# Kernel tuning notes

Hardware: AMD Instinct MI355X
Metric: run time of the kernel (lower is better)

Reference implementation:

```python
import jax, jax.numpy as jnp
import numpy as np

T, B, D, H = 512, 64, 256, 256


def setup_inputs() -> dict:
    key = jax.random.key(0)
    ks = jax.random.split(key, 14)
    w = lambda k, shp: (0.01 * jax.random.normal(k, shp, dtype=jnp.float32))
    return {
        "X": jax.random.normal(ks[0], (T, B, D), dtype=jnp.float32),
        "Wa_x": w(ks[1], (D, H)), "Wi_x": w(ks[2], (D, H)),
        "Wf_x": w(ks[3], (D, H)), "Wo_x": w(ks[4], (D, H)),
        "Wa_h": w(ks[5], (H, H)), "Wi_h": w(ks[6], (H, H)),
        "Wf_h": w(ks[7], (H, H)), "Wo_h": w(ks[8], (H, H)),
        "ba": w(ks[9], (H,)), "bi": w(ks[10], (H,)),
        "bf": w(ks[11], (H,)), "bo": w(ks[12], (H,)),
    }


def reference(X, Wa_x, Wi_x, Wf_x, Wo_x, Wa_h, Wi_h, Wf_h, Wo_h, ba, bi, bf, bo):
    # Fuse the four gate input projections into one big GEMM over all timesteps.
    # Gate order: a (cell candidate, tanh), i, f, o (sigmoid).
    h_dim = Wa_h.shape[0]
    Wx = jnp.concatenate([Wa_x, Wi_x, Wf_x, Wo_x], axis=1)      # [D, 4H]
    Wh = jnp.concatenate([Wa_h, Wi_h, Wf_h, Wo_h], axis=1)      # [H, 4H]
    b = jnp.concatenate([ba, bi, bf, bo])                        # [4H]
    gx = jnp.einsum('tbd,dg->tbg', X, Wx) + b                    # [T, B, 4H]

    def step(carry, g):
        h, s = carry
        g = g + h @ Wh                                           # [B, 4H]
        a = jnp.tanh(g[:, :h_dim])
        i = jax.nn.sigmoid(g[:, h_dim:2 * h_dim])
        f = jax.nn.sigmoid(g[:, 2 * h_dim:3 * h_dim])
        o = jax.nn.sigmoid(g[:, 3 * h_dim:])
        # t==0 in the original omits h/s terms, equivalent to h0 = s0 = 0
        s = a * i + s * f
        h = jnp.tanh(s) * o
        return (h, s), h

    bsz = X.shape[1]
    h0 = jnp.zeros((bsz, h_dim), dtype=X.dtype)
    s0 = jnp.zeros((bsz, h_dim), dtype=X.dtype)
    _, outputs = jax.lax.scan(step, (h0, s0), gx)                # [T, B, H]
    return outputs
```

## Files before the change

### kernel.cpp

```cpp
#include <hip/hip_runtime.h>
#include <hip/hip_fp16.h>


#define T_STEPS 512
#define BATCH   64
#define HID     256
#define G4      1024
#define GM      (T_STEPS * BATCH)

typedef _Float16 half2_t __attribute__((ext_vector_type(2)));
typedef _Float16 f16x8   __attribute__((ext_vector_type(8)));
typedef float    f32x4   __attribute__((ext_vector_type(4)));

#define XH_OFF  0u
#define WXT_OFF 8388608u
#define GX_OFF  8912896u
#define WH8_BYTE_OFF (8650752u * 2u)

__device__ __forceinline__ float fast_sigmoid(float x) {
    return 1.0f / (1.0f + __expf(-x));
}
__device__ __forceinline__ float fast_tanh(float x) {
    return 2.0f / (1.0f + __expf(-2.0f * x)) - 1.0f;
}

__device__ __forceinline__ unsigned char sw_e4m3(float x) {
    unsigned u = __float_as_uint(x);
    unsigned s = (u >> 24) & 0x80u;
    int e = (int)((u >> 23) & 0xffu) - 127;
    unsigned m = u & 0x7fffffu;
    if (e < -6) return (unsigned char)s;
    m += 0x00080000u;
    if (m & 0x800000u) { m = 0; e += 1; }
    int E = e + 7;
    if (E > 15 || (E == 15 && (m >> 20) > 6)) { E = 15; m = 6u << 20; }
    return (unsigned char)(s | ((unsigned)E << 3) | (m >> 20));
}
template <bool HI>
__device__ __forceinline__ unsigned cvt2_fp8(float a, float b, unsigned old) {
#if __has_builtin(__builtin_amdgcn_cvt_pk_fp8_f32)
    return (unsigned)__builtin_amdgcn_cvt_pk_fp8_f32(a, b, (int)old, HI);
#else
    unsigned lo16 = (unsigned)sw_e4m3(a) | ((unsigned)sw_e4m3(b) << 8);
    return HI ? ((old & 0xFFFFu) | (lo16 << 16))
              : ((old & 0xFFFF0000u) | lo16);
#endif
}

__global__ __launch_bounds__(256) void k_prep_x(const float* __restrict__ X,
                                                _Float16* __restrict__ Xh) {
    const int i = blockIdx.x * 256 + threadIdx.x;
    float4 v = ((const float4*)X)[i];
    half2_t a; a.x = (_Float16)v.x; a.y = (_Float16)v.y;
    half2_t b; b.x = (_Float16)v.z; b.y = (_Float16)v.w;
    ((half2_t*)Xh)[2 * i]     = a;
    ((half2_t*)Xh)[2 * i + 1] = b;
}

__global__ __launch_bounds__(256) void k_prep_w(
    const float* __restrict__ Wax, const float* __restrict__ Wix,
    const float* __restrict__ Wfx, const float* __restrict__ Wox,
    _Float16* __restrict__ Wxt)
{
    const int id = blockIdx.x * 256 + threadIdx.x;
    const int k  = id >> 10;
    const int c  = id & 1023;
    const int g  = c >> 8;
    const int j  = c & 255;
    const float* src = (g == 0) ? Wax : (g == 1) ? Wix : (g == 2) ? Wfx : Wox;
    Wxt[c * 256 + k] = (_Float16)src[k * 256 + j];
}

__global__ __launch_bounds__(256) void k_prep_wfrag8(
    const float* __restrict__ Wah, const float* __restrict__ Wih,
    const float* __restrict__ Wfh, const float* __restrict__ Woh,
    unsigned char* __restrict__ Wh8)
{
    const int id  = blockIdx.x * 256 + threadIdx.x;
    const int l   = id & 63;
    const int kt  = (id >> 6) & 7;
    const int ntG = id >> 9;
    const int c   = ntG * 16 + (l & 15);
    const int u   = c >> 2;
    const int g   = c & 3;
    const int k0  = kt * 32 + (l >> 4) * 8;
    const float* W = (g == 0) ? Wah : (g == 1) ? Wih : (g == 2) ? Wfh : Woh;
    float v[8];
#pragma unroll
    for (int e = 0; e < 8; ++e)
        v[e] = W[(size_t)(k0 + e) * 256 + u] * 64.0f;
    unsigned lo = cvt2_fp8<false>(v[0], v[1], 0u);
    lo = cvt2_fp8<true>(v[2], v[3], lo);
    unsigned hi = cvt2_fp8<false>(v[4], v[5], 0u);
    hi = cvt2_fp8<true>(v[6], v[7], hi);
    uint2 pk; pk.x = lo; pk.y = hi;
    *(uint2*)(Wh8 + ((size_t)(ntG * 8 + kt) * 64 + l) * 8) = pk;
}

__global__ __launch_bounds__(256) void k_gemm(const _Float16* __restrict__ Xh,
                                              const _Float16* __restrict__ Wxt,
                                              const float* __restrict__ ba,
                                              const float* __restrict__ bi,
                                              const float* __restrict__ bf_,
                                              const float* __restrict__ bo,
                                              _Float16* __restrict__ gx)
{
    const int lane = threadIdx.x & 63, wave = threadIdx.x >> 6;
    const int rowbase = blockIdx.x * 128 + wave * 32;
    const int colbase = blockIdx.y * 64;
    const int r15 = lane & 15, kg = lane >> 4;

    f32x4 acc[2][4] = {};
    const _Float16* ap0 = Xh  + (size_t)(rowbase + r15) * 256 + kg * 8;
    const _Float16* ap1 = ap0 + 16 * 256;
    const _Float16* bp  = Wxt + (size_t)(colbase + r15) * 256 + kg * 8;

#pragma unroll
    for (int ks = 0; ks < 8; ++ks) {
        f16x8 a0 = *(const f16x8*)(ap0 + ks * 32);
        f16x8 a1 = *(const f16x8*)(ap1 + ks * 32);
        f16x8 b0 = *(const f16x8*)(bp  + ks * 32);
        f16x8 b1 = *(const f16x8*)(bp  + 16 * 256 + ks * 32);
        f16x8 b2 = *(const f16x8*)(bp  + 32 * 256 + ks * 32);
        f16x8 b3 = *(const f16x8*)(bp  + 48 * 256 + ks * 32);
        acc[0][0] = __builtin_amdgcn_mfma_f32_16x16x32_f16(a0, b0, acc[0][0], 0, 0, 0);
        acc[0][1] = __builtin_amdgcn_mfma_f32_16x16x32_f16(a0, b1, acc[0][1], 0, 0, 0);
        acc[0][2] = __builtin_amdgcn_mfma_f32_16x16x32_f16(a0, b2, acc[0][2], 0, 0, 0);
        acc[0][3] = __builtin_amdgcn_mfma_f32_16x16x32_f16(a0, b3, acc[0][3], 0, 0, 0);
        acc[1][0] = __builtin_amdgcn_mfma_f32_16x16x32_f16(a1, b0, acc[1][0], 0, 0, 0);
        acc[1][1] = __builtin_amdgcn_mfma_f32_16x16x32_f16(a1, b1, acc[1][1], 0, 0, 0);
        acc[1][2] = __builtin_amdgcn_mfma_f32_16x16x32_f16(a1, b2, acc[1][2], 0, 0, 0);
        acc[1][3] = __builtin_amdgcn_mfma_f32_16x16x32_f16(a1, b3, acc[1][3], 0, 0, 0);
    }
    float bias_n[4];
#pragma unroll
    for (int nt = 0; nt < 4; ++nt) {
        int col = colbase + nt * 16 + r15;
        bias_n[nt] = (col < 256) ? ba[col]
                   : (col < 512) ? bi[col - 256]
                   : (col < 768) ? bf_[col - 512]
                                 : bo[col - 768];
    }
#pragma unroll
    for (int mt = 0; mt < 2; ++mt)
#pragma unroll
        for (int nt = 0; nt < 4; ++nt)
#pragma unroll
            for (int r = 0; r < 4; ++r) {
                int row = rowbase + mt * 16 + kg * 4 + r;
                int col = colbase + nt * 16 + r15;
                int g   = col >> 8, j = col & 255;
                gx[(size_t)row * G4 + 4 * j + g] =
                    (_Float16)(acc[mt][nt][r] + bias_n[nt]);
            }
}


#define M8(a, bfr, acc) \
    __builtin_amdgcn_mfma_f32_16x16x32_fp8_fp8((a), (bfr), (acc), 0, 0, 0)
#define WB(n, k) (*(const long*)(Wp + ((size_t)((n) * 8 + (k)) * 64) * 8))

#define DB(n)                                                                  \
    long b##n##_0 = WB(n,0), b##n##_1 = WB(n,1), b##n##_2 = WB(n,2),           \
         b##n##_3 = WB(n,3), b##n##_4 = WB(n,4), b##n##_5 = WB(n,5),           \
         b##n##_6 = WB(n,6), b##n##_7 = WB(n,7);

#define KSTEP(k)                                                               \
    c0  = M8(a##k, b0_##k,  c0);  c1  = M8(a##k, b1_##k,  c1);                 \
    c2  = M8(a##k, b2_##k,  c2);  c3  = M8(a##k, b3_##k,  c3);                 \
    c4  = M8(a##k, b4_##k,  c4);  c5  = M8(a##k, b5_##k,  c5);                 \
    c6  = M8(a##k, b6_##k,  c6);  c7  = M8(a##k, b7_##k,  c7);                 \
    c8  = M8(a##k, b8_##k,  c8);  c9  = M8(a##k, b9_##k,  c9);                 \
    c10 = M8(a##k, b10_##k, c10); c11 = M8(a##k, b11_##k, c11);                \
    c12 = M8(a##k, b12_##k, c12); c13 = M8(a##k, b13_##k, c13);                \
    c14 = M8(a##k, b14_##k, c14); c15 = M8(a##k, b15_##k, c15);

__global__ void __launch_bounds__(256, 1)
__attribute__((amdgpu_waves_per_eu(1, 1)))
k_recur(const unsigned char* __restrict__ Wh8, const _Float16* __restrict__ gx,
        float* __restrict__ out)
{
    const int b    = blockIdx.x;
    const int tid  = threadIdx.x;
    const int lane = tid & 63;
    const int w    = tid >> 6;

    __shared__ __align__(16) float act[1024];
    __shared__ __align__(8)  unsigned char hbufs[2][256];

    float* actw = act + w * 256;
    const unsigned char* Wp = Wh8 + ((size_t)(w * 16) * 8 * 64) * 8 + lane * 8;

    DB(0)  DB(1)  DB(2)  DB(3)  DB(4)  DB(5)  DB(6)  DB(7)
    DB(8)  DB(9)  DB(10) DB(11) DB(12) DB(13) DB(14) DB(15)

    hbufs[0][tid] = 0;
    float s = 0.0f;
    const int u = w * 64 + lane;
    uint2 gcu = *(const uint2*)(gx + (size_t)b * G4 + 4 * u);
    __syncthreads();

#pragma unroll 1
    for (int t = 0; t < T_STEPS; ++t) {
        uint2 gnx; gnx.x = 0u; gnx.y = 0u;
        if (t + 1 < T_STEPS) {
            gnx = *(const uint2*)(gx + ((size_t)(t + 1) * BATCH + b) * G4 + 4 * u);
        }

        const unsigned char* hb = &hbufs[t & 1][0] + ((lane >> 4) * 8);
        long a0 = *(const long*)(hb + 0);
        long a1 = *(const long*)(hb + 32);
        long a2 = *(const long*)(hb + 64);
        long a3 = *(const long*)(hb + 96);
        long a4 = *(const long*)(hb + 128);
        long a5 = *(const long*)(hb + 160);
        long a6 = *(const long*)(hb + 192);
        long a7 = *(const long*)(hb + 224);

        f32x4 c0  = {0,0,0,0}, c1  = {0,0,0,0}, c2  = {0,0,0,0}, c3  = {0,0,0,0};
        f32x4 c4  = {0,0,0,0}, c5  = {0,0,0,0}, c6  = {0,0,0,0}, c7  = {0,0,0,0};
        f32x4 c8  = {0,0,0,0}, c9  = {0,0,0,0}, c10 = {0,0,0,0}, c11 = {0,0,0,0};
        f32x4 c12 = {0,0,0,0}, c13 = {0,0,0,0}, c14 = {0,0,0,0}, c15 = {0,0,0,0};

        KSTEP(0) KSTEP(1) KSTEP(2) KSTEP(3)
        KSTEP(4) KSTEP(5) KSTEP(6) KSTEP(7)

        if (lane < 16) {
            actw[0  * 16 + lane] = c0[0];   actw[1  * 16 + lane] = c1[0];
            actw[2  * 16 + lane] = c2[0];   actw[3  * 16 + lane] = c3[0];
            actw[4  * 16 + lane] = c4[0];   actw[5  * 16 + lane] = c5[0];
            actw[6  * 16 + lane] = c6[0];   actw[7  * 16 + lane] = c7[0];
            actw[8  * 16 + lane] = c8[0];   actw[9  * 16 + lane] = c9[0];
            actw[10 * 16 + lane] = c10[0];  actw[11 * 16 + lane] = c11[0];
            actw[12 * 16 + lane] = c12[0];  actw[13 * 16 + lane] = c13[0];
            actw[14 * 16 + lane] = c14[0];  actw[15 * 16 + lane] = c15[0];
        }
        asm volatile("s_waitcnt lgkmcnt(0)" ::: "memory");

        {
            half2_t p01, p23;
            __builtin_memcpy(&p01, &gcu.x, 4);
            __builtin_memcpy(&p23, &gcu.y, 4);
            float4 g4v = ((const float4*)act)[w * 64 + lane];
            const float S = 0.0009765625f;
            float gA = g4v.x * S + (float)p01.x;
            float gB = g4v.y * S + (float)p01.y;
            float gC = g4v.z * S + (float)p23.x;
            float gD = g4v.w * S + (float)p23.y;
            float aa = fast_tanh(gA);
            float ii = fast_sigmoid(gB);
            float ff = fast_sigmoid(gC);
            float oo = fast_sigmoid(gD);
            s = aa * ii + s * ff;
            float h = fast_tanh(s) * oo;
            out[((size_t)t * BATCH + b) * HID + u] = h;
            unsigned p8 = cvt2_fp8<false>(h * 16.0f, h * 16.0f, 0u);
            hbufs[(t + 1) & 1][u] = (unsigned char)(p8 & 0xffu);
        }
        gcu = gnx;
        __syncthreads();
    }
}

extern "C" void kernel_launch(void* const* d_in, const int* in_sizes, int n_in,
                              void* d_out, int out_size, void* d_ws, size_t ws_size,
                              hipStream_t stream) {
    const float* X   = (const float*)d_in[0];
    const float* Wax = (const float*)d_in[1];
    const float* Wix = (const float*)d_in[2];
    const float* Wfx = (const float*)d_in[3];
    const float* Wox = (const float*)d_in[4];
    const float* Wah = (const float*)d_in[5];
    const float* Wih = (const float*)d_in[6];
    const float* Wfh = (const float*)d_in[7];
    const float* Woh = (const float*)d_in[8];
    const float* ba  = (const float*)d_in[9];
    const float* bi  = (const float*)d_in[10];
    const float* bf  = (const float*)d_in[11];
    const float* bo  = (const float*)d_in[12];

    _Float16* ws  = (_Float16*)d_ws;
    _Float16* Xh  = ws + XH_OFF;
    _Float16* Wxt = ws + WXT_OFF;
    _Float16* gxp = ws + GX_OFF;
    unsigned char* Wh8 = (unsigned char*)d_ws + WH8_BYTE_OFF;

    k_prep_x<<<dim3(GM * 256 / 4 / 256), dim3(256), 0, stream>>>(X, Xh);
    k_prep_w<<<dim3(1024), dim3(256), 0, stream>>>(Wax, Wix, Wfx, Wox, Wxt);
    k_prep_wfrag8<<<dim3(128), dim3(256), 0, stream>>>(Wah, Wih, Wfh, Woh, Wh8);
    k_gemm<<<dim3(GM / 128, G4 / 64), dim3(256), 0, stream>>>(
        Xh, Wxt, ba, bi, bf, bo, gxp);
    k_recur<<<dim3(BATCH), dim3(256), 0, stream>>>(Wh8, gxp, (float*)d_out);
}
```

Before: 929.4 us.

## Split recurrent matvec across eight waves with eight N-tiles each

The recurrent kernel goes from 4 to 8 waves per block. Each wave now holds 8 instead of 16 register-resident FP8 weight tiles and issues half as many MFMAs per timestep, which shortens the serial critical path of each step. The cost is an extra block-wide barrier per step, since gate pre-activations written by one wave are read by threads of another. Only the first 256 threads run the elementwise LSTM update, so half the block idles during that phase.

```diff
diff --git a/kernel.cpp b/kernel.cpp
--- a/kernel.cpp
+++ b/kernel.cpp
@@ -166,17 +166,13 @@
          b##n##_6 = WB(n,6), b##n##_7 = WB(n,7);
 
 #define KSTEP(k)                                                               \
-    c0  = M8(a##k, b0_##k,  c0);  c1  = M8(a##k, b1_##k,  c1);                 \
-    c2  = M8(a##k, b2_##k,  c2);  c3  = M8(a##k, b3_##k,  c3);                 \
-    c4  = M8(a##k, b4_##k,  c4);  c5  = M8(a##k, b5_##k,  c5);                 \
-    c6  = M8(a##k, b6_##k,  c6);  c7  = M8(a##k, b7_##k,  c7);                 \
-    c8  = M8(a##k, b8_##k,  c8);  c9  = M8(a##k, b9_##k,  c9);                 \
-    c10 = M8(a##k, b10_##k, c10); c11 = M8(a##k, b11_##k, c11);                \
-    c12 = M8(a##k, b12_##k, c12); c13 = M8(a##k, b13_##k, c13);                \
-    c14 = M8(a##k, b14_##k, c14); c15 = M8(a##k, b15_##k, c15);
-
-__global__ void __launch_bounds__(256, 1)
-__attribute__((amdgpu_waves_per_eu(1, 1)))
+    c0 = M8(a##k, b0_##k, c0);  c1 = M8(a##k, b1_##k, c1);                     \
+    c2 = M8(a##k, b2_##k, c2);  c3 = M8(a##k, b3_##k, c3);                     \
+    c4 = M8(a##k, b4_##k, c4);  c5 = M8(a##k, b5_##k, c5);                     \
+    c6 = M8(a##k, b6_##k, c6);  c7 = M8(a##k, b7_##k, c7);
+
+__global__ void __launch_bounds__(512, 1)
+__attribute__((amdgpu_waves_per_eu(2, 2)))
 k_recur(const unsigned char* __restrict__ Wh8, const _Float16* __restrict__ gx,
         float* __restrict__ out)
 {
@@ -188,23 +184,22 @@
     __shared__ __align__(16) float act[1024];
     __shared__ __align__(8)  unsigned char hbufs[2][256];
 
-    float* actw = act + w * 256;
-    const unsigned char* Wp = Wh8 + ((size_t)(w * 16) * 8 * 64) * 8 + lane * 8;
-
-    DB(0)  DB(1)  DB(2)  DB(3)  DB(4)  DB(5)  DB(6)  DB(7)
-    DB(8)  DB(9)  DB(10) DB(11) DB(12) DB(13) DB(14) DB(15)
-
-    hbufs[0][tid] = 0;
+    const unsigned char* Wp = Wh8 + ((size_t)(w * 8) * 8 * 64) * 8 + lane * 8;
+
+    DB(0) DB(1) DB(2) DB(3) DB(4) DB(5) DB(6) DB(7)
+
+    if (tid < 256) hbufs[0][tid] = 0;
     float s = 0.0f;
-    const int u = w * 64 + lane;
-    uint2 gcu = *(const uint2*)(gx + (size_t)b * G4 + 4 * u);
+    uint2 gcu; gcu.x = 0u; gcu.y = 0u;
+    if (tid < 256)
+        gcu = *(const uint2*)(gx + (size_t)b * G4 + 4 * tid);
     __syncthreads();
 
 #pragma unroll 1
     for (int t = 0; t < T_STEPS; ++t) {
         uint2 gnx; gnx.x = 0u; gnx.y = 0u;
-        if (t + 1 < T_STEPS) {
-            gnx = *(const uint2*)(gx + ((size_t)(t + 1) * BATCH + b) * G4 + 4 * u);
+        if (tid < 256 && t + 1 < T_STEPS) {
+            gnx = *(const uint2*)(gx + ((size_t)(t + 1) * BATCH + b) * G4 + 4 * tid);
         }
 
         const unsigned char* hb = &hbufs[t & 1][0] + ((lane >> 4) * 8);
@@ -217,31 +212,29 @@
         long a6 = *(const long*)(hb + 192);
         long a7 = *(const long*)(hb + 224);
 
-        f32x4 c0  = {0,0,0,0}, c1  = {0,0,0,0}, c2  = {0,0,0,0}, c3  = {0,0,0,0};
-        f32x4 c4  = {0,0,0,0}, c5  = {0,0,0,0}, c6  = {0,0,0,0}, c7  = {0,0,0,0};
-        f32x4 c8  = {0,0,0,0}, c9  = {0,0,0,0}, c10 = {0,0,0,0}, c11 = {0,0,0,0};
-        f32x4 c12 = {0,0,0,0}, c13 = {0,0,0,0}, c14 = {0,0,0,0}, c15 = {0,0,0,0};
+        f32x4 c0 = {0,0,0,0}, c1 = {0,0,0,0}, c2 = {0,0,0,0}, c3 = {0,0,0,0};
+        f32x4 c4 = {0,0,0,0}, c5 = {0,0,0,0}, c6 = {0,0,0,0}, c7 = {0,0,0,0};
 
         KSTEP(0) KSTEP(1) KSTEP(2) KSTEP(3)
         KSTEP(4) KSTEP(5) KSTEP(6) KSTEP(7)
 
         if (lane < 16) {
-            actw[0  * 16 + lane] = c0[0];   actw[1  * 16 + lane] = c1[0];
-            actw[2  * 16 + lane] = c2[0];   actw[3  * 16 + lane] = c3[0];
-            actw[4  * 16 + lane] = c4[0];   actw[5  * 16 + lane] = c5[0];
-            actw[6  * 16 + lane] = c6[0];   actw[7  * 16 + lane] = c7[0];
-            actw[8  * 16 + lane] = c8[0];   actw[9  * 16 + lane] = c9[0];
-            actw[10 * 16 + lane] = c10[0];  actw[11 * 16 + lane] = c11[0];
-            actw[12 * 16 + lane] = c12[0];  actw[13 * 16 + lane] = c13[0];
-            actw[14 * 16 + lane] = c14[0];  actw[15 * 16 + lane] = c15[0];
+            act[(w * 8 + 0) * 16 + lane] = c0[0];
+            act[(w * 8 + 1) * 16 + lane] = c1[0];
+            act[(w * 8 + 2) * 16 + lane] = c2[0];
+            act[(w * 8 + 3) * 16 + lane] = c3[0];
+            act[(w * 8 + 4) * 16 + lane] = c4[0];
+            act[(w * 8 + 5) * 16 + lane] = c5[0];
+            act[(w * 8 + 6) * 16 + lane] = c6[0];
+            act[(w * 8 + 7) * 16 + lane] = c7[0];
         }
-        asm volatile("s_waitcnt lgkmcnt(0)" ::: "memory");
-
-        {
+        __syncthreads();
+
+        if (tid < 256) {
             half2_t p01, p23;
             __builtin_memcpy(&p01, &gcu.x, 4);
             __builtin_memcpy(&p23, &gcu.y, 4);
-            float4 g4v = ((const float4*)act)[w * 64 + lane];
+            float4 g4v = ((const float4*)act)[tid];
             const float S = 0.0009765625f;
             float gA = g4v.x * S + (float)p01.x;
             float gB = g4v.y * S + (float)p01.y;
@@ -253,9 +246,9 @@
             float oo = fast_sigmoid(gD);
             s = aa * ii + s * ff;
             float h = fast_tanh(s) * oo;
-            out[((size_t)t * BATCH + b) * HID + u] = h;
+            out[((size_t)t * BATCH + b) * HID + tid] = h;
             unsigned p8 = cvt2_fp8<false>(h * 16.0f, h * 16.0f, 0u);
-            hbufs[(t + 1) & 1][u] = (unsigned char)(p8 & 0xffu);
+            hbufs[(t + 1) & 1][tid] = (unsigned char)(p8 & 0xffu);
         }
         gcu = gnx;
         __syncthreads();
@@ -290,5 +283,5 @@
     k_prep_wfrag8<<<dim3(128), dim3(256), 0, stream>>>(Wah, Wih, Wfh, Woh, Wh8);
     k_gemm<<<dim3(GM / 128, G4 / 64), dim3(256), 0, stream>>>(
         Xh, Wxt, ba, bi, bf, bo, gxp);
-    k_recur<<<dim3(BATCH), dim3(256), 0, stream>>>(Wh8, gxp, (float*)d_out);
-}
+    k_recur<<<dim3(BATCH), dim3(512), 0, stream>>>(Wh8, gxp, (float*)d_out);
+}
```

After: 845.0 us, median of 2. -9.1%, faster.
